# Kernel tuning notes

Measured on AMD Instinct MI355X. Metric: run time of the kernel, lower is better.

## Reference

```python
import jax, jax.numpy as jnp
import numpy as np

B, T, U, D, INNER, VOCAB = 4, 256, 64, 512, 512, 2048

def setup_inputs() -> dict:
    key = jax.random.key(0)
    ks = jax.random.split(key, 6)
    return {
        "enc_state": jax.random.normal(ks[0], (B, T, D), jnp.float32),
        "dec_state": jax.random.normal(ks[1], (B, U, D), jnp.float32),
        "W1": jax.random.normal(ks[2], (2 * D, INNER), jnp.float32) * 0.02,
        "b1": jax.random.normal(ks[3], (INNER,), jnp.float32) * 0.02,
        "W2": jax.random.normal(ks[4], (INNER, VOCAB), jnp.float32) * 0.02,
        "b2": jax.random.normal(ks[5], (VOCAB,), jnp.float32) * 0.02,
    }

def reference(enc_state, dec_state, W1, b1, W2, b2):
    # concat([enc, dec]) @ W1 == enc @ W1[:D] + dec @ W1[D:]  (same math,
    # avoids materializing the [B,T,U,2D] repeat+cat tensor)
    d = enc_state.shape[-1]
    We, Wd = W1[:d], W1[d:]
    enc_proj = jnp.einsum('btd,dk->btk', enc_state, We)           # [B,T,INNER]
    dec_proj = jnp.einsum('bud,dk->buk', dec_state, Wd)           # [B,U,INNER]
    hidden = jnp.tanh(enc_proj[:, :, None, :] + dec_proj[:, None, :, :] + b1)  # [B,T,U,INNER]
    logits = jnp.einsum('btuk,kv->btuv', hidden, W2) + b2          # [B,T,U,VOCAB]
    return logits
```

## Files before the change

### kernel.cpp

```cpp
#include <hip/hip_runtime.h>
#include <hip/hip_bf16.h>

#define B_  4
#define T_  256
#define U_  64
#define D_  512
#define INNER_ 512
#define VOCAB_ 2048

typedef __attribute__((ext_vector_type(8))) short short8;
typedef __attribute__((ext_vector_type(4))) float f32x4;

__global__ __launch_bounds__(256) void proj_kernel(
    const float* __restrict__ enc, const float* __restrict__ dec,
    const float* __restrict__ W1, const float* __restrict__ b1,
    float* __restrict__ encP, float* __restrict__ decPb) {
  int ct = blockIdx.x;
  int rt = blockIdx.y;
  const float* src; float* dst; int kOff; int addB1; int rowBase;
  if (rt < 64) { src = enc; dst = encP; kOff = 0; addB1 = 0; rowBase = rt * 16; }
  else { src = dec; dst = decPb; kOff = D_; addB1 = 1; rowBase = (rt - 64) * 16; }

  __shared__ float As[16][D_];
  int tid = threadIdx.x;
  const float4* s4 = (const float4*)(src + (size_t)rowBase * D_);
  float4* a4 = (float4*)(&As[0][0]);
#pragma unroll
  for (int i = 0; i < 8; i++) a4[tid + 256 * i] = s4[tid + 256 * i];
  __syncthreads();

  int colQ = (tid & 31) * 4;
  int col = ct * 128 + colQ;
  int r0 = (tid >> 5) * 2;
  float a00=0,a01=0,a02=0,a03=0, a10=0,a11=0,a12=0,a13=0;
  const float* Wp = W1 + (size_t)kOff * INNER_ + col;
#pragma unroll 4
  for (int k = 0; k < D_; k++) {
    float4 w = *(const float4*)(Wp + (size_t)k * INNER_);
    float e0 = As[r0][k], e1 = As[r0 + 1][k];
    a00 += e0 * w.x; a01 += e0 * w.y; a02 += e0 * w.z; a03 += e0 * w.w;
    a10 += e1 * w.x; a11 += e1 * w.y; a12 += e1 * w.z; a13 += e1 * w.w;
  }
  float4 bb = {0,0,0,0};
  if (addB1) bb = *(const float4*)(b1 + col);
  float4 o0 = {a00 + bb.x, a01 + bb.y, a02 + bb.z, a03 + bb.w};
  float4 o1 = {a10 + bb.x, a11 + bb.y, a12 + bb.z, a13 + bb.w};
  *(float4*)(dst + (size_t)(rowBase + r0) * INNER_ + col) = o0;
  *(float4*)(dst + (size_t)(rowBase + r0 + 1) * INNER_ + col) = o1;
}

__global__ __launch_bounds__(256) void w2t_kernel(
    const float* __restrict__ W2, __hip_bfloat16* __restrict__ W2T) {
  __shared__ float tile[32][33];
  int vBase = blockIdx.x * 32;
  int kBase = blockIdx.y * 32;
  int tx = threadIdx.x & 31, ty = threadIdx.x >> 5;
#pragma unroll
  for (int i = 0; i < 32; i += 8)
    tile[ty + i][tx] = W2[(size_t)(kBase + ty + i) * VOCAB_ + vBase + tx];
  __syncthreads();
#pragma unroll
  for (int i = 0; i < 32; i += 8)
    W2T[(size_t)(vBase + ty + i) * INNER_ + kBase + tx] = __float2bfloat16(tile[tx][ty + i]);
}

__global__ __launch_bounds__(256) void hidden_kernel(
    const float* __restrict__ encP, const float* __restrict__ decPb,
    __hip_bfloat16* __restrict__ H) {
  int gid = blockIdx.x * 256 + threadIdx.x;
  int k0 = (gid & 63) * 8;
  int r = gid >> 6;
  int u = r & 63;
  int bt = r >> 6;
  int b = bt >> 8;
  const float4* e = (const float4*)(encP + (size_t)bt * 512 + k0);
  const float4* dv = (const float4*)(decPb + (size_t)(b * 64 + u) * 512 + k0);
  float4 e0 = e[0], e1 = e[1];
  float4 d0 = dv[0], d1 = dv[1];
  union { __hip_bfloat16 h[8]; uint4 v; } p;
  p.h[0] = __float2bfloat16(tanhf(e0.x + d0.x));
  p.h[1] = __float2bfloat16(tanhf(e0.y + d0.y));
  p.h[2] = __float2bfloat16(tanhf(e0.z + d0.z));
  p.h[3] = __float2bfloat16(tanhf(e0.w + d0.w));
  p.h[4] = __float2bfloat16(tanhf(e1.x + d1.x));
  p.h[5] = __float2bfloat16(tanhf(e1.y + d1.y));
  p.h[6] = __float2bfloat16(tanhf(e1.z + d1.z));
  p.h[7] = __float2bfloat16(tanhf(e1.w + d1.w));
  *(uint4*)((__hip_bfloat16*)H + (size_t)r * 512 + k0) = p.v;
}

__device__ inline void gload_lds16(const void* g, void* l) {
  __builtin_amdgcn_global_load_lds(
      (const __attribute__((address_space(1))) unsigned int*)g,
      (__attribute__((address_space(3))) unsigned int*)l, 16, 0, 0);
}

__global__ __launch_bounds__(512, 2) void joint_gemm(
    const __hip_bfloat16* __restrict__ H, const __hip_bfloat16* __restrict__ W2T,
    const float* __restrict__ b2, float* __restrict__ out) {
  extern __shared__ char smem[];
  int tid = threadIdx.x;
  int lane = tid & 63, wave = tid >> 6;
  int wm = wave >> 2, wn = wave & 3;

  int bid = blockIdx.x;
  int wg = (bid & 7) * 256 + (bid >> 3);
  int rt = wg >> 3;
  int ct = wg & 7;
  size_t rowBase = (size_t)rt * 256;
  int colBase = ct * 256;

  int srow = tid >> 3;
  int kswz = ((tid & 7) ^ (srow & 7)) * 8;
  const __hip_bfloat16* pA = H   + (rowBase + srow) * 512 + kswz;
  const __hip_bfloat16* pB = W2T + (size_t)(colBase + srow) * 512 + kswz;
  __hip_bfloat16* ldsA = (__hip_bfloat16*)smem;
  __hip_bfloat16* ldsB = (__hip_bfloat16*)(smem + 65536);
  int stageRow = wave * 8;

#define STAGE(t, buf) do {                                                    \
    const __hip_bfloat16* ga = pA + (size_t)(t) * 64;                         \
    const __hip_bfloat16* gb = pB + (size_t)(t) * 64;                         \
    __hip_bfloat16* la = ldsA + (buf) * 16384 + stageRow * 64;                \
    __hip_bfloat16* lb = ldsB + (buf) * 16384 + stageRow * 64;                \
    _Pragma("unroll")                                                         \
    for (int j = 0; j < 4; j++) {                                             \
      gload_lds16(ga + (size_t)j * 64 * 512, la + j * 64 * 64);               \
      gload_lds16(gb + (size_t)j * 64 * 512, lb + j * 64 * 64);               \
    } } while (0)

  int lrA = wm * 128 + (lane & 15);
  int lrB = wn * 64 + (lane & 15);
  int sx = (lane & 7) * 16;
  int q16 = (lane >> 4) * 16;
  int offA0 = lrA * 128 + (q16 ^ sx);
  int offA1 = lrA * 128 + ((64 + q16) ^ sx);
  int offB0 = lrB * 128 + (q16 ^ sx);
  int offB1 = lrB * 128 + ((64 + q16) ^ sx);

  float bv[4];
#pragma unroll
  for (int ni = 0; ni < 4; ni++) bv[ni] = b2[colBase + wn * 64 + ni * 16 + (lane & 15)];
  f32x4 acc[8][4];
#pragma unroll
  for (int mi = 0; mi < 8; mi++)
#pragma unroll
    for (int ni = 0; ni < 4; ni++)
      acc[mi][ni] = (f32x4){bv[ni], bv[ni], bv[ni], bv[ni]};

  asm volatile("s_waitcnt vmcnt(0)" ::: "memory");
  __builtin_amdgcn_sched_barrier(0);

  STAGE(0, 0);
  STAGE(1, 1);

#define KITER(t, buf, VMC, DOSTAGE) do {                                      \
    asm volatile("s_waitcnt vmcnt(" #VMC ")" ::: "memory");                   \
    __builtin_amdgcn_sched_barrier(0);                                        \
    __builtin_amdgcn_s_barrier();                                             \
    __builtin_amdgcn_sched_barrier(0);                                        \
    const char* baA = (const char*)ldsA + (buf) * 32768;                      \
    const char* baB = (const char*)ldsB + (buf) * 32768;                      \
    short8 bfr[4][2], afr[4][2];                                              \
    _Pragma("unroll") for (int ni = 0; ni < 4; ni++) {                        \
      bfr[ni][0] = *(const short8*)(baB + offB0 + ni * 2048);                 \
      bfr[ni][1] = *(const short8*)(baB + offB1 + ni * 2048); }               \
    _Pragma("unroll") for (int mi = 0; mi < 4; mi++) {                        \
      afr[mi][0] = *(const short8*)(baA + offA0 + mi * 2048);                 \
      afr[mi][1] = *(const short8*)(baA + offA1 + mi * 2048); }               \
    __builtin_amdgcn_s_setprio(1);                                            \
    _Pragma("unroll") for (int mi = 0; mi < 4; mi++)                          \
      _Pragma("unroll") for (int ni = 0; ni < 4; ni++) {                      \
        acc[mi][ni] = __builtin_amdgcn_mfma_f32_16x16x32_bf16(                \
            afr[mi][0], bfr[ni][0], acc[mi][ni], 0, 0, 0);                    \
        acc[mi][ni] = __builtin_amdgcn_mfma_f32_16x16x32_bf16(                \
            afr[mi][1], bfr[ni][1], acc[mi][ni], 0, 0, 0); }                  \
    __builtin_amdgcn_s_setprio(0);                                            \
    _Pragma("unroll") for (int mi = 0; mi < 4; mi++) {                        \
      afr[mi][0] = *(const short8*)(baA + offA0 + 8192 + mi * 2048);          \
      afr[mi][1] = *(const short8*)(baA + offA1 + 8192 + mi * 2048); }        \
    asm volatile("s_waitcnt lgkmcnt(0)" ::: "memory");                        \
    __builtin_amdgcn_sched_barrier(0);                                        \
    __builtin_amdgcn_s_barrier();                                             \
    __builtin_amdgcn_sched_barrier(0);                                        \
    if (DOSTAGE) { STAGE((t) + 2, (buf)); }                                   \
    __builtin_amdgcn_sched_barrier(0);                                        \
    __builtin_amdgcn_s_setprio(1);                                            \
    _Pragma("unroll") for (int mi = 0; mi < 4; mi++)                          \
      _Pragma("unroll") for (int ni = 0; ni < 4; ni++) {                      \
        acc[mi + 4][ni] = __builtin_amdgcn_mfma_f32_16x16x32_bf16(            \
            afr[mi][0], bfr[ni][0], acc[mi + 4][ni], 0, 0, 0);                \
        acc[mi + 4][ni] = __builtin_amdgcn_mfma_f32_16x16x32_bf16(            \
            afr[mi][1], bfr[ni][1], acc[mi + 4][ni], 0, 0, 0); }              \
    __builtin_amdgcn_s_setprio(0);                                            \
  } while (0)

#pragma unroll 2
  for (int t = 0; t < 6; ++t) KITER(t, (t & 1), 8, 1);
  KITER(6, 0, 8, 0);
  KITER(7, 1, 0, 0);
#undef KITER
#undef STAGE

  {
    float* lp = (float*)smem;
    float* outBase = out + rowBase * VOCAB_ + colBase;
#pragma unroll
    for (int r = 0; r < 4; r++) {
      __syncthreads();
      if (wm == (r >> 1)) {
        int mih = (r & 1) * 4;
#pragma unroll
        for (int q = 0; q < 4; q++) {
          int lrow0 = q * 16 + ((lane >> 4) << 2);
#pragma unroll
          for (int ni = 0; ni < 4; ni++) {
            int col = wn * 64 + ni * 16 + (lane & 15);
            f32x4 v = acc[mih + q][ni];
#pragma unroll
            for (int j = 0; j < 4; j++)
              lp[(lrow0 + j) * 260 + col] = v[j];
          }
        }
      }
      __syncthreads();
#pragma unroll
      for (int i = 0; i < 8; i++) {
        int c = tid + 512 * i;
        int row = c >> 6, cc = c & 63;
        f32x4 v = *(const f32x4*)(lp + row * 260 + cc * 4);
        *(float4*)(outBase + (size_t)(r * 64 + row) * VOCAB_ + cc * 4) =
            (float4){v[0], v[1], v[2], v[3]};
      }
    }
  }
}

extern "C" void kernel_launch(void* const* d_in, const int* in_sizes, int n_in,
                              void* d_out, int out_size, void* d_ws, size_t ws_size,
                              hipStream_t stream) {
  const float* enc = (const float*)d_in[0];
  const float* dec = (const float*)d_in[1];
  const float* W1  = (const float*)d_in[2];
  const float* b1  = (const float*)d_in[3];
  const float* W2  = (const float*)d_in[4];
  const float* b2  = (const float*)d_in[5];
  float* out = (float*)d_out;

  char* ws = (char*)d_ws;
  float* encP  = (float*)ws;
  float* decPb = (float*)(ws + (2u << 20));
  __hip_bfloat16* W2T = (__hip_bfloat16*)(ws + (2u << 20) + (512u << 10));
  __hip_bfloat16* H   = (__hip_bfloat16*)(ws + (2u << 20) + (512u << 10) + (2u << 20));

  static int smem_set = 0;
  if (!smem_set) {
    (void)hipFuncSetAttribute((const void*)joint_gemm,
                              hipFuncAttributeMaxDynamicSharedMemorySize, 131072);
    smem_set = 1;
  }

  proj_kernel<<<dim3(4, 80), 256, 0, stream>>>(enc, dec, W1, b1, encP, decPb);
  w2t_kernel<<<dim3(64, 16), 256, 0, stream>>>(W2, W2T);
  hidden_kernel<<<16384, 256, 0, stream>>>(encP, decPb, H);
  joint_gemm<<<dim3(2048), 512, 131072, stream>>>(H, W2T, b2, out);
}
```

Before: 724.7 us.

## Shrink joint GEMM block tile to 256x128 with 256 threads and K-step 32

The bf16 joint GEMM block tile shrinks from 256x256 with 8 waves to 256x128 with 4 waves. The K-step drops from 64 to 32, giving 16 iterations, and the LDS swizzle and fragment offsets are rebuilt for 32-wide rows. Each wave still computes a 128x64 sub-tile. Dynamic LDS falls from 128KB to 48KB, so several blocks can be resident per CU and overlap each other's loads, MFMA work and epilogue stores. The cost is more loads of the H matrix from global memory, because each A row block is now fetched once for every 128 output columns instead of every 256.

```diff
diff --git a/kernel.cpp b/kernel.cpp
--- a/kernel.cpp
+++ b/kernel.cpp
@@ -95,48 +95,44 @@
       (__attribute__((address_space(3))) unsigned int*)l, 16, 0, 0);
 }
 
-__global__ __launch_bounds__(512, 2) void joint_gemm(
+__global__ __launch_bounds__(256, 2) void joint_gemm(
     const __hip_bfloat16* __restrict__ H, const __hip_bfloat16* __restrict__ W2T,
     const float* __restrict__ b2, float* __restrict__ out) {
   extern __shared__ char smem[];
   int tid = threadIdx.x;
   int lane = tid & 63, wave = tid >> 6;
-  int wm = wave >> 2, wn = wave & 3;
+  int wm = wave >> 1, wn = wave & 1;
 
   int bid = blockIdx.x;
-  int wg = (bid & 7) * 256 + (bid >> 3);
-  int rt = wg >> 3;
-  int ct = wg & 7;
+  int wg = (bid & 7) * 512 + (bid >> 3);
+  int rt = wg >> 4;
+  int ct = wg & 15;
   size_t rowBase = (size_t)rt * 256;
-  int colBase = ct * 256;
-
-  int srow = tid >> 3;
-  int kswz = ((tid & 7) ^ (srow & 7)) * 8;
+  int colBase = ct * 128;
+
+  int srow = tid >> 2;
+  int kswz = ((tid & 3) ^ ((tid >> 3) & 3)) * 8;
   const __hip_bfloat16* pA = H   + (rowBase + srow) * 512 + kswz;
   const __hip_bfloat16* pB = W2T + (size_t)(colBase + srow) * 512 + kswz;
-  __hip_bfloat16* ldsA = (__hip_bfloat16*)smem;
-  __hip_bfloat16* ldsB = (__hip_bfloat16*)(smem + 65536);
-  int stageRow = wave * 8;
+  char* ldsA = smem;
+  char* ldsB = smem + 32768;
 
 #define STAGE(t, buf) do {                                                    \
-    const __hip_bfloat16* ga = pA + (size_t)(t) * 64;                         \
-    const __hip_bfloat16* gb = pB + (size_t)(t) * 64;                         \
-    __hip_bfloat16* la = ldsA + (buf) * 16384 + stageRow * 64;                \
-    __hip_bfloat16* lb = ldsB + (buf) * 16384 + stageRow * 64;                \
+    const __hip_bfloat16* ga = pA + (size_t)(t) * 32;                         \
+    const __hip_bfloat16* gb = pB + (size_t)(t) * 32;                         \
+    char* la = ldsA + (buf) * 16384 + wave * 1024;                            \
+    char* lb = ldsB + (buf) * 8192 + wave * 1024;                             \
     _Pragma("unroll")                                                         \
-    for (int j = 0; j < 4; j++) {                                             \
-      gload_lds16(ga + (size_t)j * 64 * 512, la + j * 64 * 64);               \
-      gload_lds16(gb + (size_t)j * 64 * 512, lb + j * 64 * 64);               \
-    } } while (0)
-
-  int lrA = wm * 128 + (lane & 15);
-  int lrB = wn * 64 + (lane & 15);
-  int sx = (lane & 7) * 16;
-  int q16 = (lane >> 4) * 16;
-  int offA0 = lrA * 128 + (q16 ^ sx);
-  int offA1 = lrA * 128 + ((64 + q16) ^ sx);
-  int offB0 = lrB * 128 + (q16 ^ sx);
-  int offB1 = lrB * 128 + ((64 + q16) ^ sx);
+    for (int j = 0; j < 4; j++)                                               \
+      gload_lds16(ga + (size_t)j * 64 * 512, la + j * 4096);                  \
+    _Pragma("unroll")                                                         \
+    for (int j = 0; j < 2; j++)                                               \
+      gload_lds16(gb + (size_t)j * 64 * 512, lb + j * 4096);                  \
+  } while (0)
+
+  int laneOff = (lane & 15) * 64 + (((lane >> 4) ^ (((lane & 15) >> 1) & 3)) * 16);
+  int offA = wm * 8192 + laneOff;
+  int offB = wn * 4096 + laneOff;
 
   float bv[4];
 #pragma unroll
@@ -159,46 +155,31 @@
     __builtin_amdgcn_sched_barrier(0);                                        \
     __builtin_amdgcn_s_barrier();                                             \
     __builtin_amdgcn_sched_barrier(0);                                        \
-    const char* baA = (const char*)ldsA + (buf) * 32768;                      \
-    const char* baB = (const char*)ldsB + (buf) * 32768;                      \
-    short8 bfr[4][2], afr[4][2];                                              \
-    _Pragma("unroll") for (int ni = 0; ni < 4; ni++) {                        \
-      bfr[ni][0] = *(const short8*)(baB + offB0 + ni * 2048);                 \
-      bfr[ni][1] = *(const short8*)(baB + offB1 + ni * 2048); }               \
-    _Pragma("unroll") for (int mi = 0; mi < 4; mi++) {                        \
-      afr[mi][0] = *(const short8*)(baA + offA0 + mi * 2048);                 \
-      afr[mi][1] = *(const short8*)(baA + offA1 + mi * 2048); }               \
+    const char* baA = ldsA + (buf) * 16384;                                   \
+    const char* baB = ldsB + (buf) * 8192;                                    \
+    short8 afr[8], bfr[4];                                                    \
+    _Pragma("unroll") for (int ni = 0; ni < 4; ni++)                          \
+      bfr[ni] = *(const short8*)(baB + offB + ni * 1024);                     \
+    _Pragma("unroll") for (int mi = 0; mi < 8; mi++)                          \
+      afr[mi] = *(const short8*)(baA + offA + mi * 1024);                     \
+    asm volatile("s_waitcnt lgkmcnt(0)" ::: "memory");                        \
+    __builtin_amdgcn_sched_barrier(0);                                        \
+    __builtin_amdgcn_s_barrier();                                             \
+    __builtin_amdgcn_sched_barrier(0);                                        \
+    if (DOSTAGE) { STAGE((t) + 2, (buf)); }                                   \
+    __builtin_amdgcn_sched_barrier(0);                                        \
     __builtin_amdgcn_s_setprio(1);                                            \
-    _Pragma("unroll") for (int mi = 0; mi < 4; mi++)                          \
-      _Pragma("unroll") for (int ni = 0; ni < 4; ni++) {                      \
+    _Pragma("unroll") for (int mi = 0; mi < 8; mi++)                          \
+      _Pragma("unroll") for (int ni = 0; ni < 4; ni++)                        \
         acc[mi][ni] = __builtin_amdgcn_mfma_f32_16x16x32_bf16(                \
-            afr[mi][0], bfr[ni][0], acc[mi][ni], 0, 0, 0);                    \
-        acc[mi][ni] = __builtin_amdgcn_mfma_f32_16x16x32_bf16(                \
-            afr[mi][1], bfr[ni][1], acc[mi][ni], 0, 0, 0); }                  \
-    __builtin_amdgcn_s_setprio(0);                                            \
-    _Pragma("unroll") for (int mi = 0; mi < 4; mi++) {                        \
-      afr[mi][0] = *(const short8*)(baA + offA0 + 8192 + mi * 2048);          \
-      afr[mi][1] = *(const short8*)(baA + offA1 + 8192 + mi * 2048); }        \
-    asm volatile("s_waitcnt lgkmcnt(0)" ::: "memory");                        \
-    __builtin_amdgcn_sched_barrier(0);                                        \
-    __builtin_amdgcn_s_barrier();                                             \
-    __builtin_amdgcn_sched_barrier(0);                                        \
-    if (DOSTAGE) { STAGE((t) + 2, (buf)); }                                   \
-    __builtin_amdgcn_sched_barrier(0);                                        \
-    __builtin_amdgcn_s_setprio(1);                                            \
-    _Pragma("unroll") for (int mi = 0; mi < 4; mi++)                          \
-      _Pragma("unroll") for (int ni = 0; ni < 4; ni++) {                      \
-        acc[mi + 4][ni] = __builtin_amdgcn_mfma_f32_16x16x32_bf16(            \
-            afr[mi][0], bfr[ni][0], acc[mi + 4][ni], 0, 0, 0);                \
-        acc[mi + 4][ni] = __builtin_amdgcn_mfma_f32_16x16x32_bf16(            \
-            afr[mi][1], bfr[ni][1], acc[mi + 4][ni], 0, 0, 0); }              \
+            afr[mi], bfr[ni], acc[mi][ni], 0, 0, 0);                          \
     __builtin_amdgcn_s_setprio(0);                                            \
   } while (0)
 
 #pragma unroll 2
-  for (int t = 0; t < 6; ++t) KITER(t, (t & 1), 8, 1);
-  KITER(6, 0, 8, 0);
-  KITER(7, 1, 0, 0);
+  for (int t = 0; t < 14; ++t) KITER(t, (t & 1), 6, 1);
+  KITER(14, 0, 6, 0);
+  KITER(15, 1, 0, 0);
 #undef KITER
 #undef STAGE
 
@@ -219,16 +200,16 @@
             f32x4 v = acc[mih + q][ni];
 #pragma unroll
             for (int j = 0; j < 4; j++)
-              lp[(lrow0 + j) * 260 + col] = v[j];
+              lp[(lrow0 + j) * 132 + col] = v[j];
           }
         }
       }
       __syncthreads();
 #pragma unroll
       for (int i = 0; i < 8; i++) {
-        int c = tid + 512 * i;
-        int row = c >> 6, cc = c & 63;
-        f32x4 v = *(const f32x4*)(lp + row * 260 + cc * 4);
+        int c = tid + 256 * i;
+        int row = c >> 5, cc = c & 31;
+        f32x4 v = *(const f32x4*)(lp + row * 132 + cc * 4);
         *(float4*)(outBase + (size_t)(r * 64 + row) * VOCAB_ + cc * 4) =
             (float4){v[0], v[1], v[2], v[3]};
       }
@@ -256,12 +237,12 @@
   static int smem_set = 0;
   if (!smem_set) {
     (void)hipFuncSetAttribute((const void*)joint_gemm,
-                              hipFuncAttributeMaxDynamicSharedMemorySize, 131072);
+                              hipFuncAttributeMaxDynamicSharedMemorySize, 49152);
     smem_set = 1;
   }
 
   proj_kernel<<<dim3(4, 80), 256, 0, stream>>>(enc, dec, W1, b1, encP, decPb);
   w2t_kernel<<<dim3(64, 16), 256, 0, stream>>>(W2, W2T);
   hidden_kernel<<<16384, 256, 0, stream>>>(encP, decPb, H);
-  joint_gemm<<<dim3(2048), 512, 131072, stream>>>(H, W2T, b2, out);
-}
+  joint_gemm<<<dim3(4096), 256, 49152, stream>>>(H, W2T, b2, out);
+}
```

After: 728.9 us. Within noise of the previous version (+0.6%).
